# Kernel tuning notes

Measured on AMD Instinct MI355X. Metric: run time of the kernel, lower is better.

## Reference

```python
import jax, jax.numpy as jnp
import numpy as np

S, B, D = 2048, 2, 1024   # seq_len, batch, d_model
H, Dh = 16, 64            # n_head, d_head (H*Dh == D)
LN_EPS = 1e-5


def _rel_shift(x):
    # x: [qlen, klen, bsz, n_head] -- standard Transformer-XL relative shift
    q, k, b, n = x.shape
    x = jnp.pad(x, ((0, 0), (1, 0), (0, 0), (0, 0)))  # [q, k+1, b, n]
    x = x.reshape(k + 1, q, b, n)[1:]                  # drop first row
    return x.reshape(q, k, b, n)


def setup_inputs() -> dict:
    key = jax.random.key(0)
    ks = jax.random.split(key, 8)
    s = 0.02
    return {
        "x":    jax.random.normal(ks[0], (S, B, D), jnp.float32),
        "r":    jax.random.normal(ks[1], (1, D), jnp.float32),          # learned pos vector
        "rw":   jax.random.normal(ks[2], (H, Dh), jnp.float32),          # content bias
        "rr":   jax.random.normal(ks[3], (H, Dh), jnp.float32),          # position bias
        "ln_g": jnp.ones((D,), jnp.float32),
        "ln_b": jnp.zeros((D,), jnp.float32),
        "Wqkv": jax.random.normal(ks[4], (D, 3 * H * Dh), jnp.float32) * s,
        "Wr":   jax.random.normal(ks[5], (D, H * Dh), jnp.float32) * s,
        "Wo":   jax.random.normal(ks[6], (H * Dh, D), jnp.float32) * s,
    }


def reference(x, r, rw, rr, ln_g, ln_b, Wqkv, Wr, Wo):
    # Pre-LayerNorm (dropout = identity in eval mode)
    mu = jnp.mean(x, axis=-1, keepdims=True)
    var = jnp.mean(jnp.square(x - mu), axis=-1, keepdims=True)
    xn = (x - mu) * jax.lax.rsqrt(var + LN_EPS) * ln_g + ln_b   # [S,B,D]

    # relative position input: r expanded over seq
    r_exp = jnp.broadcast_to(r, (S, D))                          # [S,D]

    qkv = xn @ Wqkv                                              # [S,B,3*H*Dh]
    q, k, v = jnp.split(qkv, 3, axis=-1)
    q = q.reshape(S, B, H, Dh)
    k = k.reshape(S, B, H, Dh)
    v = v.reshape(S, B, H, Dh)
    rk = (r_exp @ Wr).reshape(S, H, Dh)                          # [S,H,Dh]

    scale = 1.0 / np.sqrt(Dh).astype(np.float32)
    AC = jnp.einsum('ibnd,jbnd->ijbn', q + rw, k)                # content term
    BD = jnp.einsum('ibnd,jnd->ijbn', q + rr, rk)                # position term
    BD = _rel_shift(BD)
    attn = jax.nn.softmax((AC + BD) * scale, axis=1)             # over key axis j

    av = jnp.einsum('ijbn,jbnd->ibnd', attn, v).reshape(S, B, H * Dh)
    return xn + av @ Wo                                          # residual w/ normed input
```

## Files before the change

kernel.cpp:

```cpp
#include <hip/hip_runtime.h>

typedef unsigned short u16;
typedef __attribute__((ext_vector_type(8))) __bf16 bf16x8;
typedef __attribute__((ext_vector_type(8))) u16 u16x8;
typedef __attribute__((ext_vector_type(4))) float f32x4;
typedef __attribute__((ext_vector_type(16))) float f32x16;

__device__ __forceinline__ float bf2f(u16 u){
  union { unsigned int i; float f; } v; v.i = ((unsigned int)u) << 16; return v.f;
}
__device__ __forceinline__ u16 f2bf(float f){
  union { float f; unsigned int u; } v; v.f = f;
  unsigned int u = v.u;
  u += 0x7FFFu + ((u >> 16) & 1u);
  return (u16)(u >> 16);
}
__device__ __forceinline__ unsigned fbits(float f){
  union { float f; unsigned u; } v; v.f = f; return v.u;
}
__device__ __forceinline__ void gld_lds16(const u16* g, u16* l){
  __builtin_amdgcn_global_load_lds((const __attribute__((address_space(1))) unsigned int*)g,
                                   (__attribute__((address_space(3))) unsigned int*)l, 16, 0, 0);
}

__global__ __launch_bounds__(256) void transpose_k(const float* __restrict__ in, u16* __restrict__ out,
                                                   int R, int C){
  __shared__ float tile[32][33];
  const int bx = blockIdx.x * 32, by = blockIdx.y * 32;
  const int tx = threadIdx.x, ty = threadIdx.y;
  #pragma unroll
  for(int i = 0; i < 32; i += 8)
    tile[ty + i][tx] = in[(size_t)(by + ty + i) * C + bx + tx];
  __syncthreads();
  #pragma unroll
  for(int i = 0; i < 32; i += 8)
    out[(size_t)(bx + ty + i) * R + by + tx] = f2bf(tile[tx][ty + i]);
}

__global__ __launch_bounds__(256) void ln_k(const float* __restrict__ x, const float* __restrict__ gw,
                                            const float* __restrict__ bw, u16* __restrict__ xnb){
  const int row = blockIdx.x, t = threadIdx.x;
  const float* xr = x + (size_t)row * 1024;
  float4 xv = *reinterpret_cast<const float4*>(xr + t * 4);
  float s  = xv.x + xv.y + xv.z + xv.w;
  float s2 = xv.x*xv.x + xv.y*xv.y + xv.z*xv.z + xv.w*xv.w;
  #pragma unroll
  for(int m = 1; m <= 32; m <<= 1){ s += __shfl_xor(s, m, 64); s2 += __shfl_xor(s2, m, 64); }
  __shared__ float red[8];
  const int w = t >> 6, lane = t & 63;
  if(lane == 0){ red[w] = s; red[4 + w] = s2; }
  __syncthreads();
  float S1 = red[0] + red[1] + red[2] + red[3];
  float S2 = red[4] + red[5] + red[6] + red[7];
  float mu = S1 * (1.f/1024.f);
  float var = S2 * (1.f/1024.f) - mu * mu;
  float rstd = rsqrtf(var + 1e-5f);
  float4 gv = *reinterpret_cast<const float4*>(gw + t * 4);
  float4 bv = *reinterpret_cast<const float4*>(bw + t * 4);
  ushort4 o;
  o.x = f2bf((xv.x - mu) * rstd * gv.x + bv.x);
  o.y = f2bf((xv.y - mu) * rstd * gv.y + bv.y);
  o.z = f2bf((xv.z - mu) * rstd * gv.z + bv.z);
  o.w = f2bf((xv.w - mu) * rstd * gv.w + bv.w);
  *reinterpret_cast<ushort4*>(xnb + (size_t)row * 1024 + t * 4) = o;
}

__global__ __launch_bounds__(256) void rk0_k(const float* __restrict__ r, const float* __restrict__ Wr,
                                             float* __restrict__ rk0){
  const int n = blockIdx.x * 256 + threadIdx.x;
  const int d0 = blockIdx.y * 128;
  float acc = 0.f;
  for(int d = d0; d < d0 + 128; ++d)
    acc += r[d] * Wr[(size_t)d * 1024 + n];
  atomicAdd(&rk0[n], acc);
}

__global__ __launch_bounds__(256) void c_k(const u16* __restrict__ qk, const float* __restrict__ rr,
                                           const float* __restrict__ rk0, float* __restrict__ cc){
  const int w = threadIdx.x >> 6, lane = threadIdx.x & 63;
  const int ib = blockIdx.x * 4 + w;
  const u16* qp = qk + (size_t)ib * 2048 + lane * 16;
  u16x8 q0 = *reinterpret_cast<const u16x8*>(qp);
  u16x8 q1 = *reinterpret_cast<const u16x8*>(qp + 8);
  const float* rrp = rr + lane * 16;
  const float* rkp = rk0 + lane * 16;
  float s = 0.f;
  #pragma unroll
  for(int e = 0; e < 8; ++e){
    s += (bf2f(q0[e]) + rrp[e]) * rkp[e];
    s += (bf2f(q1[e]) + rrp[8 + e]) * rkp[8 + e];
  }
  s += __shfl_xor(s, 1, 64);
  s += __shfl_xor(s, 2, 64);
  if((lane & 3) == 0) cc[(size_t)ib * 16 + (lane >> 2)] = s;
}

__global__ __launch_bounds__(256) void vtrans_k(const u16* __restrict__ vnat, u16* __restrict__ vT){
  __shared__ u16 tl[128][40];
  const int t = threadIdx.x;
  const int i0 = blockIdx.x * 128, c0 = blockIdx.y * 32, b = blockIdx.z;
  {
    const int ii = t & 127, cs = (t >> 7) * 16;
    const u16* p = vnat + (size_t)((i0 + ii) * 2 + b) * 1024 + c0 + cs;
    *reinterpret_cast<u16x8*>(&tl[ii][cs])     = *reinterpret_cast<const u16x8*>(p);
    *reinterpret_cast<u16x8*>(&tl[ii][cs + 8]) = *reinterpret_cast<const u16x8*>(p + 8);
  }
  __syncthreads();
  const int dr = t & 31, seg = t >> 5;
  const int R = (b * 16 + (c0 >> 6)) * 64 + (c0 & 63) + dr;
  u16 tmp[16];
  #pragma unroll
  for(int e = 0; e < 16; ++e) tmp[e] = tl[seg * 16 + e][dr];
  u16* op = vT + (size_t)R * 2048 + i0 + seg * 16;
  *reinterpret_cast<u16x8*>(op)     = *reinterpret_cast<u16x8*>(&tmp[0]);
  *reinterpret_cast<u16x8*>(op + 8) = *reinterpret_cast<u16x8*>(&tmp[8]);
}

template<int MODE>
__global__ __launch_bounds__(256) void gemm_bt_k(const u16* __restrict__ A, const u16* __restrict__ BT,
                                                 const u16* __restrict__ res, u16* __restrict__ Cb,
                                                 float* __restrict__ Cf, u16* __restrict__ vnat,
                                                 int M, int N, int K){
  __shared__ u16 sA[128 * 32];
  __shared__ u16 sB[128 * 32];
  const int t = threadIdx.x;
  const int row0 = blockIdx.y * 128, col0 = blockIdx.x * 128;
  const int w = t >> 6, lane = t & 63, g = lane >> 4, lq = lane & 15;
  const int wr = (w >> 1) * 64, wc = (w & 1) * 64;
  const int s0 = t, s1 = t + 256;
  f32x4 zero4 = {0.f, 0.f, 0.f, 0.f};
  f32x4 acc[4][4];
  #pragma unroll
  for(int mi = 0; mi < 4; ++mi)
    #pragma unroll
    for(int ni = 0; ni < 4; ++ni) acc[mi][ni] = zero4;

  for(int kt = 0; kt < K; kt += 32){
    gld_lds16(A  + (size_t)(row0 + (s0 >> 2)) * K + kt + (s0 & 3) * 8, &sA[w * 512]);
    gld_lds16(A  + (size_t)(row0 + (s1 >> 2)) * K + kt + (s1 & 3) * 8, &sA[2048 + w * 512]);
    gld_lds16(BT + (size_t)(col0 + (s0 >> 2)) * K + kt + (s0 & 3) * 8, &sB[w * 512]);
    gld_lds16(BT + (size_t)(col0 + (s1 >> 2)) * K + kt + (s1 & 3) * 8, &sB[2048 + w * 512]);
    __syncthreads();
    bf16x8 af[4];
    #pragma unroll
    for(int mi = 0; mi < 4; ++mi)
      af[mi] = *reinterpret_cast<const bf16x8*>(&sA[(wr + mi * 16 + lq) * 32 + g * 8]);
    #pragma unroll
    for(int ni = 0; ni < 4; ++ni){
      bf16x8 bfr = *reinterpret_cast<const bf16x8*>(&sB[(wc + ni * 16 + lq) * 32 + g * 8]);
      #pragma unroll
      for(int mi = 0; mi < 4; ++mi)
        acc[mi][ni] = __builtin_amdgcn_mfma_f32_16x16x32_bf16(af[mi], bfr, acc[mi][ni], 0, 0, 0);
    }
    __syncthreads();
  }
  #pragma unroll
  for(int mi = 0; mi < 4; ++mi)
    #pragma unroll
    for(int ni = 0; ni < 4; ++ni)
      #pragma unroll
      for(int rg = 0; rg < 4; ++rg){
        const int row = row0 + wr + mi * 16 + g * 4 + rg;
        const int col = col0 + wc + ni * 16 + lq;
        float v = acc[mi][ni][rg];
        if(MODE == 1){
          v += bf2f(res[(size_t)row * N + col]);
          Cf[(size_t)row * N + col] = v;
        } else {
          if(col < 2048) Cb[(size_t)row * 2048 + col] = f2bf(v);
          else           vnat[(size_t)row * 1024 + (col - 2048)] = f2bf(v);
        }
      }
}

__global__ __launch_bounds__(256) void attn_k(const u16* __restrict__ qk, const u16* __restrict__ vT,
                                              const float* __restrict__ rw, const float* __restrict__ cc,
                                              u16* __restrict__ av){
  constexpr int S = 2048, ST = 74;
  __shared__ u16 ks[2][64 * ST];
  __shared__ u16 vs[2][64 * ST];
  const int t = threadIdx.x;
  const int i0 = blockIdx.x * 128;
  const int bh = blockIdx.y;
  const int b = bh >> 4, h = bh & 15;
  const int w = t >> 6, lane = t & 63, m = lane & 31, q5 = lane >> 5;
  const int iw0 = i0 + w * 32;
  const int i_lane = iw0 + m;
  const float SC = 0.125f * 1.4426950408889634f;

  bf16x8 qf[4];
  {
    const u16* qp = qk + (size_t)(i_lane * 2 + b) * 2048 + h * 64;
    const float* rwp = rw + h * 64;
    #pragma unroll
    for(int kt = 0; kt < 4; ++kt){
      const int dbase = kt * 16 + q5 * 8;
      u16x8 qv = *reinterpret_cast<const u16x8*>(qp + dbase);
      u16x8 a;
      #pragma unroll
      for(int e = 0; e < 8; ++e) a[e] = f2bf((bf2f(qv[e]) + rwp[dbase + e]) * SC);
      qf[kt] = *reinterpret_cast<bf16x8*>(&a);
    }
  }
  const float ciL = cc[(size_t)(i_lane * 2 + b) * 16 + h] * SC;
  const float cpL = (i_lane + 1 < S) ? cc[(size_t)((i_lane + 1) * 2 + b) * 16 + h] * SC : 0.0f;

  f32x16 acc0, acc1, z16;
  #pragma unroll
  for(int e = 0; e < 16; ++e) z16[e] = 0.f;
  acc0 = z16; acc1 = z16;
  float rsum = 0.f;

  const int jr = t >> 2, c0 = (t & 3) * 16;
  {
    const u16* kp = qk + (size_t)(jr * 2 + b) * 2048 + 1024 + h * 64 + c0;
    *reinterpret_cast<u16x8*>(&ks[0][jr * ST + c0])     = *reinterpret_cast<const u16x8*>(kp);
    *reinterpret_cast<u16x8*>(&ks[0][jr * ST + c0 + 8]) = *reinterpret_cast<const u16x8*>(kp + 8);
    const u16* vp = vT + ((size_t)bh * 64 + jr) * 2048 + c0;
    *reinterpret_cast<u16x8*>(&vs[0][jr * ST + c0])     = *reinterpret_cast<const u16x8*>(vp);
    *reinterpret_cast<u16x8*>(&vs[0][jr * ST + c0 + 8]) = *reinterpret_cast<const u16x8*>(vp + 8);
  }
  __syncthreads();

  for(int n = 0; n < 32; ++n){
    const int p = n & 1;
    u16x8 k0, k1, v0, v1;
    const bool pre = (n + 1 < 32);
    if(pre){
      const int j0n = (n + 1) * 64;
      const u16* kp = qk + (size_t)((j0n + jr) * 2 + b) * 2048 + 1024 + h * 64 + c0;
      k0 = *reinterpret_cast<const u16x8*>(kp);
      k1 = *reinterpret_cast<const u16x8*>(kp + 8);
      const u16* vp = vT + ((size_t)bh * 64 + jr) * 2048 + j0n + c0;
      v0 = *reinterpret_cast<const u16x8*>(vp);
      v1 = *reinterpret_cast<const u16x8*>(vp + 8);
    }
    const int j0 = n * 64;
    bf16x8 pfrag[4];
    #pragma unroll
    for(int jt = 0; jt < 2; ++jt){
      const int tj0 = j0 + jt * 32;
      f32x16 s = z16;
      #pragma unroll
      for(int kt = 0; kt < 4; ++kt){
        bf16x8 ka = *reinterpret_cast<const bf16x8*>(&ks[p][(jt * 32 + m) * ST + kt * 16 + q5 * 8]);
        s = __builtin_amdgcn_mfma_f32_32x32x16_bf16(ka, qf[kt], s, 0, 0, 0);
      }
      float pv[16];
      if(tj0 + 31 <= iw0){
        #pragma unroll
        for(int r = 0; r < 16; ++r) pv[r] = __builtin_amdgcn_exp2f(s[r] + ciL);
      } else if(tj0 >= iw0 + 33){
        #pragma unroll
        for(int r = 0; r < 16; ++r) pv[r] = __builtin_amdgcn_exp2f(s[r] + cpL);
      } else {
        #pragma unroll
        for(int r = 0; r < 16; ++r){
          const int j = tj0 + (r & 3) + 8 * (r >> 2) + 4 * q5;
          const float t1 = (j <= i_lane) ? ciL : cpL;
          const float bdL = (j == i_lane + 1) ? 0.0f : t1;
          pv[r] = __builtin_amdgcn_exp2f(s[r] + bdL);
        }
      }
      #pragma unroll
      for(int r = 0; r < 16; ++r) rsum += pv[r];
      unsigned pk[8];
      #pragma unroll
      for(int q = 0; q < 8; ++q)
        pk[q] = __builtin_amdgcn_perm(fbits(pv[2 * q + 1]), fbits(pv[2 * q]), 0x07060302);
      unsigned sAx = (q5 == 0) ? pk[2] : pk[0];
      unsigned sAy = (q5 == 0) ? pk[3] : pk[1];
      unsigned rAx = (unsigned)__shfl_xor((int)sAx, 32, 64);
      unsigned rAy = (unsigned)__shfl_xor((int)sAy, 32, 64);
      unsigned sBx = (q5 == 0) ? pk[6] : pk[4];
      unsigned sBy = (q5 == 0) ? pk[7] : pk[5];
      unsigned rBx = (unsigned)__shfl_xor((int)sBx, 32, 64);
      unsigned rBy = (unsigned)__shfl_xor((int)sBy, 32, 64);
      union { unsigned u[4]; bf16x8 bf; } f0, f1;
      if(q5 == 0){
        f0.u[0] = pk[0]; f0.u[1] = pk[1]; f0.u[2] = rAx; f0.u[3] = rAy;
        f1.u[0] = pk[4]; f1.u[1] = pk[5]; f1.u[2] = rBx; f1.u[3] = rBy;
      } else {
        f0.u[0] = rAx; f0.u[1] = rAy; f0.u[2] = pk[2]; f0.u[3] = pk[3];
        f1.u[0] = rBx; f1.u[1] = rBy; f1.u[2] = pk[6]; f1.u[3] = pk[7];
      }
      pfrag[jt * 2 + 0] = f0.bf;
      pfrag[jt * 2 + 1] = f1.bf;
    }
    #pragma unroll
    for(int kt = 0; kt < 4; ++kt){
      bf16x8 va0 = *reinterpret_cast<const bf16x8*>(&vs[p][(m) * ST + kt * 16 + q5 * 8]);
      acc0 = __builtin_amdgcn_mfma_f32_32x32x16_bf16(va0, pfrag[kt], acc0, 0, 0, 0);
      bf16x8 va1 = *reinterpret_cast<const bf16x8*>(&vs[p][(32 + m) * ST + kt * 16 + q5 * 8]);
      acc1 = __builtin_amdgcn_mfma_f32_32x32x16_bf16(va1, pfrag[kt], acc1, 0, 0, 0);
    }
    if(pre){
      const int q2 = p ^ 1;
      *reinterpret_cast<u16x8*>(&ks[q2][jr * ST + c0])     = k0;
      *reinterpret_cast<u16x8*>(&ks[q2][jr * ST + c0 + 8]) = k1;
      *reinterpret_cast<u16x8*>(&vs[q2][jr * ST + c0])     = v0;
      *reinterpret_cast<u16x8*>(&vs[q2][jr * ST + c0 + 8]) = v1;
    }
    __syncthreads();
  }
  rsum += __shfl_xor(rsum, 32, 64);
  const float rinv = 1.0f / rsum;
  u16* op = av + (size_t)(i_lane * 2 + b) * 1024 + h * 64;
  #pragma unroll
  for(int dt = 0; dt < 2; ++dt){
    const f32x16& A = dt ? acc1 : acc0;
    #pragma unroll
    for(int rq = 0; rq < 4; ++rq){
      ushort4 o;
      o.x = f2bf(A[rq * 4 + 0] * rinv);
      o.y = f2bf(A[rq * 4 + 1] * rinv);
      o.z = f2bf(A[rq * 4 + 2] * rinv);
      o.w = f2bf(A[rq * 4 + 3] * rinv);
      const int d0 = dt * 32 + 8 * rq + 4 * q5;
      *reinterpret_cast<ushort4*>(op + d0) = o;
    }
  }
}

extern "C" void kernel_launch(void* const* d_in, const int* in_sizes, int n_in,
                              void* d_out, int out_size, void* d_ws, size_t ws_size,
                              hipStream_t stream){
  (void)in_sizes; (void)n_in; (void)out_size; (void)ws_size;
  const float* x    = (const float*)d_in[0];
  const float* r    = (const float*)d_in[1];
  const float* rw   = (const float*)d_in[2];
  const float* rr   = (const float*)d_in[3];
  const float* ln_g = (const float*)d_in[4];
  const float* ln_b = (const float*)d_in[5];
  const float* Wqkv = (const float*)d_in[6];
  const float* Wr   = (const float*)d_in[7];
  const float* Wo   = (const float*)d_in[8];
  char* ws = (char*)d_ws;
  u16*   xnb   = (u16*)(ws + 0);
  u16*   qk    = (u16*)(ws + 8388608);
  u16*   av    = (u16*)(ws + 25165824);
  u16*   woT   = (u16*)(ws + 33554432);
  u16*   wqkvT = (u16*)(ws + 35651584);
  u16*   vT    = (u16*)(ws + 41943040);
  float* rk0   = (float*)(ws + 50331648);
  float* cc    = (float*)(ws + 50335744);
  u16*   vnat  = av;
  float* out   = (float*)d_out;

  transpose_k<<<dim3(96, 32), dim3(32, 8), 0, stream>>>(Wqkv, wqkvT, 1024, 3072);
  transpose_k<<<dim3(32, 32), dim3(32, 8), 0, stream>>>(Wo, woT, 1024, 1024);
  ln_k<<<4096, 256, 0, stream>>>(x, ln_g, ln_b, xnb);
  hipMemsetAsync(rk0, 0, 4096, stream);
  rk0_k<<<dim3(4, 8), 256, 0, stream>>>(r, Wr, rk0);
  gemm_bt_k<2><<<dim3(24, 32), 256, 0, stream>>>(xnb, wqkvT, nullptr, qk, nullptr, vnat, 4096, 3072, 1024);
  vtrans_k<<<dim3(16, 32, 2), 256, 0, stream>>>(vnat, vT);
  c_k<<<1024, 256, 0, stream>>>(qk, rr, rk0, cc);
  attn_k<<<dim3(16, 32), 256, 0, stream>>>(qk, vT, rw, cc, av);
  gemm_bt_k<1><<<dim3(8, 32), 256, 0, stream>>>(av, woT, xnb, nullptr, out, nullptr, 4096, 1024, 1024);
}
```

Baseline: 236.0 us.

## Merge weight transposes, fold memset, deepen QKV GEMM K-step, retile output GEMM

Combines the two weight-transpose launches into one kernel that also zeroes the rk0 accumulator, which removes a launch and the memset. The rk0 reduction gets more blocks with shorter loops. The QKV GEMM now loads two 32-wide K slices per barrier pair, halving the synchronisation count, and its epilogue branches per block instead of per element. The output GEMM uses 128x64 tiles to double the block count for better CU occupancy, at the cost of less B reuse.

```diff
diff --git a/kernel.cpp b/kernel.cpp
--- a/kernel.cpp
+++ b/kernel.cpp
@@ -23,11 +23,20 @@
                                    (__attribute__((address_space(3))) unsigned int*)l, 16, 0, 0);
 }
 
-__global__ __launch_bounds__(256) void transpose_k(const float* __restrict__ in, u16* __restrict__ out,
-                                                   int R, int C){
+__global__ __launch_bounds__(256) void transpose2_k(const float* __restrict__ Wqkv, u16* __restrict__ wqkvT,
+                                                    const float* __restrict__ Wo, u16* __restrict__ woT,
+                                                    float* __restrict__ rk0z){
   __shared__ float tile[32][33];
-  const int bx = blockIdx.x * 32, by = blockIdx.y * 32;
   const int tx = threadIdx.x, ty = threadIdx.y;
+  const float* in; u16* out; int C, bxx;
+  if(blockIdx.x < 96){ in = Wqkv; out = wqkvT; C = 3072; bxx = blockIdx.x; }
+  else               { in = Wo;   out = woT;   C = 1024; bxx = blockIdx.x - 96; }
+  const int R = 1024;
+  if(blockIdx.x == 0 && blockIdx.y == 0){
+    float4 z = {0.f, 0.f, 0.f, 0.f};
+    reinterpret_cast<float4*>(rk0z)[ty * 32 + tx] = z;
+  }
+  const int bx = bxx * 32, by = blockIdx.y * 32;
   #pragma unroll
   for(int i = 0; i < 32; i += 8)
     tile[ty + i][tx] = in[(size_t)(by + ty + i) * C + bx + tx];
@@ -68,9 +77,9 @@
 __global__ __launch_bounds__(256) void rk0_k(const float* __restrict__ r, const float* __restrict__ Wr,
                                              float* __restrict__ rk0){
   const int n = blockIdx.x * 256 + threadIdx.x;
-  const int d0 = blockIdx.y * 128;
+  const int d0 = blockIdx.y * 32;
   float acc = 0.f;
-  for(int d = d0; d < d0 + 128; ++d)
+  for(int d = d0; d < d0 + 32; ++d)
     acc += r[d] * Wr[(size_t)d * 1024 + n];
   atomicAdd(&rk0[n], acc);
 }
@@ -116,18 +125,15 @@
   *reinterpret_cast<u16x8*>(op + 8) = *reinterpret_cast<u16x8*>(&tmp[8]);
 }
 
-template<int MODE>
-__global__ __launch_bounds__(256) void gemm_bt_k(const u16* __restrict__ A, const u16* __restrict__ BT,
-                                                 const u16* __restrict__ res, u16* __restrict__ Cb,
-                                                 float* __restrict__ Cf, u16* __restrict__ vnat,
-                                                 int M, int N, int K){
-  __shared__ u16 sA[128 * 32];
-  __shared__ u16 sB[128 * 32];
+__global__ __launch_bounds__(256) void gemm_qkv_k(const u16* __restrict__ A, const u16* __restrict__ BT,
+                                                  u16* __restrict__ Cb, u16* __restrict__ vnat){
+  __shared__ u16 sA[2][128 * 32];
+  __shared__ u16 sB[2][128 * 32];
   const int t = threadIdx.x;
   const int row0 = blockIdx.y * 128, col0 = blockIdx.x * 128;
   const int w = t >> 6, lane = t & 63, g = lane >> 4, lq = lane & 15;
   const int wr = (w >> 1) * 64, wc = (w & 1) * 64;
-  const int s0 = t, s1 = t + 256;
+  const int K = 1024;
   f32x4 zero4 = {0.f, 0.f, 0.f, 0.f};
   f32x4 acc[4][4];
   #pragma unroll
@@ -135,18 +141,84 @@
     #pragma unroll
     for(int ni = 0; ni < 4; ++ni) acc[mi][ni] = zero4;
 
+  for(int kt = 0; kt < K; kt += 64){
+    #pragma unroll
+    for(int ks = 0; ks < 2; ++ks){
+      const int kk = kt + ks * 32;
+      gld_lds16(A  + (size_t)(row0 +      (t >> 2)) * K + kk + (t & 3) * 8, &sA[ks][w * 512]);
+      gld_lds16(A  + (size_t)(row0 + 64 + (t >> 2)) * K + kk + (t & 3) * 8, &sA[ks][2048 + w * 512]);
+      gld_lds16(BT + (size_t)(col0 +      (t >> 2)) * K + kk + (t & 3) * 8, &sB[ks][w * 512]);
+      gld_lds16(BT + (size_t)(col0 + 64 + (t >> 2)) * K + kk + (t & 3) * 8, &sB[ks][2048 + w * 512]);
+    }
+    __syncthreads();
+    #pragma unroll
+    for(int ks = 0; ks < 2; ++ks){
+      bf16x8 af[4];
+      #pragma unroll
+      for(int mi = 0; mi < 4; ++mi)
+        af[mi] = *reinterpret_cast<const bf16x8*>(&sA[ks][(wr + mi * 16 + lq) * 32 + g * 8]);
+      #pragma unroll
+      for(int ni = 0; ni < 4; ++ni){
+        bf16x8 bfr = *reinterpret_cast<const bf16x8*>(&sB[ks][(wc + ni * 16 + lq) * 32 + g * 8]);
+        #pragma unroll
+        for(int mi = 0; mi < 4; ++mi)
+          acc[mi][ni] = __builtin_amdgcn_mfma_f32_16x16x32_bf16(af[mi], bfr, acc[mi][ni], 0, 0, 0);
+      }
+    }
+    __syncthreads();
+  }
+  if(blockIdx.x < 16){
+    #pragma unroll
+    for(int mi = 0; mi < 4; ++mi)
+      #pragma unroll
+      for(int ni = 0; ni < 4; ++ni)
+        #pragma unroll
+        for(int rg = 0; rg < 4; ++rg){
+          const int row = row0 + wr + mi * 16 + g * 4 + rg;
+          const int col = col0 + wc + ni * 16 + lq;
+          Cb[(size_t)row * 2048 + col] = f2bf(acc[mi][ni][rg]);
+        }
+  } else {
+    #pragma unroll
+    for(int mi = 0; mi < 4; ++mi)
+      #pragma unroll
+      for(int ni = 0; ni < 4; ++ni)
+        #pragma unroll
+        for(int rg = 0; rg < 4; ++rg){
+          const int row = row0 + wr + mi * 16 + g * 4 + rg;
+          const int col = col0 + wc + ni * 16 + lq - 2048;
+          vnat[(size_t)row * 1024 + col] = f2bf(acc[mi][ni][rg]);
+        }
+  }
+}
+
+__global__ __launch_bounds__(256) void gemm_out_k(const u16* __restrict__ A, const u16* __restrict__ BT,
+                                                  const u16* __restrict__ res, float* __restrict__ Cf){
+  __shared__ u16 sA[128 * 32];
+  __shared__ u16 sB[64 * 32];
+  const int t = threadIdx.x;
+  const int row0 = blockIdx.y * 128, col0 = blockIdx.x * 64;
+  const int w = t >> 6, lane = t & 63, g = lane >> 4, lq = lane & 15;
+  const int wr = (w >> 1) * 64, wc = (w & 1) * 32;
+  const int K = 1024, N = 1024;
+  f32x4 zero4 = {0.f, 0.f, 0.f, 0.f};
+  f32x4 acc[4][2];
+  #pragma unroll
+  for(int mi = 0; mi < 4; ++mi)
+    #pragma unroll
+    for(int ni = 0; ni < 2; ++ni) acc[mi][ni] = zero4;
+
   for(int kt = 0; kt < K; kt += 32){
-    gld_lds16(A  + (size_t)(row0 + (s0 >> 2)) * K + kt + (s0 & 3) * 8, &sA[w * 512]);
-    gld_lds16(A  + (size_t)(row0 + (s1 >> 2)) * K + kt + (s1 & 3) * 8, &sA[2048 + w * 512]);
-    gld_lds16(BT + (size_t)(col0 + (s0 >> 2)) * K + kt + (s0 & 3) * 8, &sB[w * 512]);
-    gld_lds16(BT + (size_t)(col0 + (s1 >> 2)) * K + kt + (s1 & 3) * 8, &sB[2048 + w * 512]);
+    gld_lds16(A  + (size_t)(row0 +      (t >> 2)) * K + kt + (t & 3) * 8, &sA[w * 512]);
+    gld_lds16(A  + (size_t)(row0 + 64 + (t >> 2)) * K + kt + (t & 3) * 8, &sA[2048 + w * 512]);
+    gld_lds16(BT + (size_t)(col0 +      (t >> 2)) * K + kt + (t & 3) * 8, &sB[w * 512]);
     __syncthreads();
     bf16x8 af[4];
     #pragma unroll
     for(int mi = 0; mi < 4; ++mi)
       af[mi] = *reinterpret_cast<const bf16x8*>(&sA[(wr + mi * 16 + lq) * 32 + g * 8]);
     #pragma unroll
-    for(int ni = 0; ni < 4; ++ni){
+    for(int ni = 0; ni < 2; ++ni){
       bf16x8 bfr = *reinterpret_cast<const bf16x8*>(&sB[(wc + ni * 16 + lq) * 32 + g * 8]);
       #pragma unroll
       for(int mi = 0; mi < 4; ++mi)
@@ -157,19 +229,12 @@
   #pragma unroll
   for(int mi = 0; mi < 4; ++mi)
     #pragma unroll
-    for(int ni = 0; ni < 4; ++ni)
+    for(int ni = 0; ni < 2; ++ni)
       #pragma unroll
       for(int rg = 0; rg < 4; ++rg){
         const int row = row0 + wr + mi * 16 + g * 4 + rg;
         const int col = col0 + wc + ni * 16 + lq;
-        float v = acc[mi][ni][rg];
-        if(MODE == 1){
-          v += bf2f(res[(size_t)row * N + col]);
-          Cf[(size_t)row * N + col] = v;
-        } else {
-          if(col < 2048) Cb[(size_t)row * 2048 + col] = f2bf(v);
-          else           vnat[(size_t)row * 1024 + (col - 2048)] = f2bf(v);
-        }
+        Cf[(size_t)row * N + col] = acc[mi][ni][rg] + bf2f(res[(size_t)row * N + col]);
       }
 }
 
@@ -347,14 +412,12 @@
   u16*   vnat  = av;
   float* out   = (float*)d_out;
 
-  transpose_k<<<dim3(96, 32), dim3(32, 8), 0, stream>>>(Wqkv, wqkvT, 1024, 3072);
-  transpose_k<<<dim3(32, 32), dim3(32, 8), 0, stream>>>(Wo, woT, 1024, 1024);
+  transpose2_k<<<dim3(128, 32), dim3(32, 8), 0, stream>>>(Wqkv, wqkvT, Wo, woT, rk0);
   ln_k<<<4096, 256, 0, stream>>>(x, ln_g, ln_b, xnb);
-  hipMemsetAsync(rk0, 0, 4096, stream);
-  rk0_k<<<dim3(4, 8), 256, 0, stream>>>(r, Wr, rk0);
-  gemm_bt_k<2><<<dim3(24, 32), 256, 0, stream>>>(xnb, wqkvT, nullptr, qk, nullptr, vnat, 4096, 3072, 1024);
+  rk0_k<<<dim3(4, 32), 256, 0, stream>>>(r, Wr, rk0);
+  gemm_qkv_k<<<dim3(24, 32), 256, 0, stream>>>(xnb, wqkvT, qk, vnat);
   vtrans_k<<<dim3(16, 32, 2), 256, 0, stream>>>(vnat, vT);
   c_k<<<1024, 256, 0, stream>>>(qk, rr, rk0, cc);
   attn_k<<<dim3(16, 32), 256, 0, stream>>>(qk, vT, rw, cc, av);
-  gemm_bt_k<1><<<dim3(8, 32), 256, 0, stream>>>(av, woT, xnb, nullptr, out, nullptr, 4096, 1024, 1024);
-}
+  gemm_out_k<<<dim3(16, 32), 256, 0, stream>>>(av, woT, xnb, out);
+}
```

New measurement: 231.1 us. 1.02x faster.
